# Optimization experiments

Hardware: AMD Instinct MI355X
Metric: run time of the kernel (lower is better)

## Reference

```python
import jax, jax.numpy as jnp
import numpy as np

B = 32768
H = 512
NH = 8
EPS = 1e-5


def _glorot(key, shape):
    fan_in, fan_out = shape[-1], shape[0]
    lim = (6.0 / (fan_in + fan_out)) ** 0.5
    return jax.random.uniform(key, shape, jnp.float32, -lim, lim)


def setup_inputs() -> dict:
    key = jax.random.key(0)
    ks = jax.random.split(key, 32)
    d = {
        "graph_features": jax.random.normal(ks[0], (B, H), jnp.float32),
        "seq_features": jax.random.normal(ks[1], (B, H), jnp.float32),
        "tabular_features": jax.random.normal(ks[2], (B, H), jnp.float32),
    }
    i = 3
    for name in ("g2s", "s2g", "t2m"):
        d[f"{name}_w_in"] = _glorot(ks[i], (3 * H, H)); i += 1
        d[f"{name}_b_in"] = jnp.zeros((3 * H,), jnp.float32)
        d[f"{name}_w_out"] = _glorot(ks[i], (H, H)); i += 1
        d[f"{name}_b_out"] = jnp.zeros((H,), jnp.float32)
    for name in ("gate_g", "gate_s", "gate_t"):
        d[f"{name}_w"] = _glorot(ks[i], (H, 2 * H)); i += 1
        d[f"{name}_b"] = jnp.zeros((H,), jnp.float32)
    d["fc1_w"] = _glorot(ks[i], (2 * H, 3 * H)); i += 1
    d["fc1_b"] = jnp.zeros((2 * H,), jnp.float32)
    d["ln_g"] = jnp.ones((2 * H,), jnp.float32)
    d["ln_b"] = jnp.zeros((2 * H,), jnp.float32)
    d["fc2_w"] = _glorot(ks[i], (H, 2 * H)); i += 1
    d["fc2_b"] = jnp.zeros((H,), jnp.float32)
    return d


def _mha(q, k, v, w_in, b_in, w_out, b_out):
    # q: [B,Sq,H], k/v: [B,Sk,H]. PyTorch nn.MultiheadAttention math (eval mode).
    dh = H // NH
    qp = q @ w_in[:H].T + b_in[:H]
    kp = k @ w_in[H:2 * H].T + b_in[H:2 * H]
    vp = v @ w_in[2 * H:].T + b_in[2 * H:]
    qh = qp.reshape(qp.shape[0], qp.shape[1], NH, dh)
    kh = kp.reshape(kp.shape[0], kp.shape[1], NH, dh)
    vh = vp.reshape(vp.shape[0], vp.shape[1], NH, dh)
    scores = jnp.einsum("bqhd,bkhd->bhqk", qh, kh) / jnp.sqrt(jnp.float32(dh))
    attn = jax.nn.softmax(scores, axis=-1)
    out = jnp.einsum("bhqk,bkhd->bqhd", attn, vh).reshape(q.shape[0], q.shape[1], H)
    return out @ w_out.T + b_out


def reference(graph_features, seq_features, tabular_features,
              g2s_w_in, g2s_b_in, g2s_w_out, g2s_b_out,
              s2g_w_in, s2g_b_in, s2g_w_out, s2g_b_out,
              t2m_w_in, t2m_b_in, t2m_w_out, t2m_b_out,
              gate_g_w, gate_g_b, gate_s_w, gate_s_b, gate_t_w, gate_t_b,
              fc1_w, fc1_b, ln_g, ln_b, fc2_w, fc2_b):
    g = graph_features[:, None, :]   # [B,1,H]
    s = seq_features[:, None, :]
    t = tabular_features[:, None, :]

    graph_to_seq = _mha(s, g, g, g2s_w_in, g2s_b_in, g2s_w_out, g2s_b_out)
    seq_to_graph = _mha(g, s, s, s2g_w_in, s2g_b_in, s2g_w_out, s2g_b_out)

    graph_gate = jax.nn.sigmoid(jnp.concatenate([g, seq_to_graph], -1) @ gate_g_w.T + gate_g_b)
    seq_gate = jax.nn.sigmoid(jnp.concatenate([s, graph_to_seq], -1) @ gate_s_w.T + gate_s_b)
    gated_graph = g * graph_gate
    gated_seq = s * seq_gate

    multimodal = jnp.concatenate([gated_graph, gated_seq], axis=1)  # [B,2,H]
    t2m = _mha(multimodal, t, t, t2m_w_in, t2m_b_in, t2m_w_out, t2m_b_out)  # [B,2,H]

    tab_comb = jnp.concatenate([t, t2m.mean(axis=1, keepdims=True)], -1)
    tab_gate = jax.nn.sigmoid(tab_comb @ gate_t_w.T + gate_t_b)
    gated_tab = t * tab_gate

    allf = jnp.concatenate([gated_graph[:, 0], gated_seq[:, 0], gated_tab[:, 0]], -1)  # [B,3H]
    h = allf @ fc1_w.T + fc1_b
    mu = h.mean(-1, keepdims=True)
    var = ((h - mu) ** 2).mean(-1, keepdims=True)
    h = (h - mu) / jnp.sqrt(var + EPS) * ln_g + ln_b
    h = jax.nn.relu(h)
    return h @ fc2_w.T + fc2_b
```

## Files before the change

### kernel.cpp

```cpp
#include <hip/hip_runtime.h>
#include <stdint.h>
#include <stddef.h>

#define MROWS 32768
#define HDIM  512
#define CH    16384
#define BM 128
#define BN 128
#define BK 64

typedef __attribute__((ext_vector_type(8))) _Float16 half8;
typedef __attribute__((ext_vector_type(4))) _Float16 half4v;
typedef __attribute__((ext_vector_type(4))) float    f32x4;

static __device__ __forceinline__ void gld_lds16(const void* g, void* l) {
    __builtin_amdgcn_global_load_lds(
        (__attribute__((address_space(1))) void*)(uintptr_t)g,
        (__attribute__((address_space(3))) void*)(uint32_t)(uintptr_t)l,
        16, 0, 0);
}

struct CvtJob  { const float* src; _Float16* dst; int srcld4, dstld, rowlen4, rows; };
struct CvtJobs { CvtJob j[11]; };

__global__ __launch_bounds__(256)
void cvt_rows(CvtJobs J) {
    const CvtJob jb = J.j[blockIdx.y];
    const int row = blockIdx.x;
    if (row >= jb.rows) return;
    const float4* __restrict__ s = (const float4*)jb.src + (size_t)row * jb.srcld4;
    _Float16* __restrict__ d = jb.dst + (size_t)row * jb.dstld;
    for (int c = threadIdx.x; c < jb.rowlen4; c += 256) {
        const float4 v = s[c];
        half4v o = { (_Float16)v.x, (_Float16)v.y, (_Float16)v.z, (_Float16)v.w };
        *(half4v*)(d + c * 4) = o;
    }
}

__global__ __launch_bounds__(384)
void cvt_chunk3(const float* __restrict__ x0, const float* __restrict__ x1,
                const float* __restrict__ x2, _Float16* __restrict__ dst) {
    const int row = blockIdx.x;
    const int mod = threadIdx.x >> 7;
    const int c   = threadIdx.x & 127;
    const float* s = (mod == 0) ? x0 : (mod == 1) ? x1 : x2;
    const float4 v = ((const float4*)(s + (size_t)row * 512))[c];
    half4v o = { (_Float16)v.x, (_Float16)v.y, (_Float16)v.z, (_Float16)v.w };
    *(half4v*)(dst + (size_t)row * 1536 + mod * 512 + c * 4) = o;
}

struct TcvtArgs { const float* src[3]; _Float16* dst; };
__global__ __launch_bounds__(256)
void tcvt512(TcvtArgs a) {
    __shared__ float t[32][33];
    const int m = blockIdx.z;
    const float* __restrict__ src = a.src[m];
    _Float16* __restrict__ dst = a.dst + (size_t)m * HDIM * HDIM;
    const int bx = blockIdx.x * 32, by = blockIdx.y * 32;
    const int tx = threadIdx.x & 31, ty = threadIdx.x >> 5;
    #pragma unroll
    for (int q = 0; q < 4; ++q)
        t[ty + q * 8][tx] = src[(size_t)(by + ty + q * 8) * 512 + bx + tx];
    __syncthreads();
    #pragma unroll
    for (int q = 0; q < 4; ++q)
        dst[(size_t)(bx + ty + q * 8) * 512 + by + tx] = (_Float16)t[tx][ty + q * 8];
}

struct MvArgs { const float* W[3]; const float* x[3]; const float* b[3]; float* y; int ldw, woff; };
__global__ __launch_bounds__(256)
void mv3(MvArgs a) {
    const int m = blockIdx.y;
    const int i = blockIdx.x * 256 + threadIdx.x;
    const float* __restrict__ W = a.W[m] + (size_t)i * a.ldw + a.woff;
    const float* __restrict__ x = a.x[m];
    float s = a.b[m][i];
    for (int j = 0; j < 512; ++j) s += W[j] * x[j];
    a.y[m * 512 + i] = s;
}

struct GemmP {
    const void* A1;
    const _Float16* W; const float* bias; void* C;
    int K, ldA1, ldw, ldc, coff;
    int zsA, zsW, zsC;
};

template<int EPI, int OCC>
__global__ __launch_bounds__(256, OCC)
void gemm_k(GemmP p) {
    __shared__ __align__(16) unsigned char smem[32768];
    _Float16* Asm = (_Float16*)smem;
    _Float16* Bsm = (_Float16*)(smem + 16384);

    const int tid  = threadIdx.x;
    const int wid  = tid >> 6;
    const int lane = tid & 63;
    const int m0 = blockIdx.x * BM;
    const int n0 = blockIdx.y * BN;
    const ptrdiff_t zz = (ptrdiff_t)blockIdx.z;
    const _Float16* __restrict__ A1h = (const _Float16*)((const char*)p.A1 + zz * p.zsA);
    const _Float16* __restrict__ Wp  = (const _Float16*)((const char*)p.W + zz * p.zsW);
    char* Cz = (char*)p.C + zz * p.zsC;

    const int wr = (wid >> 1) * 64;
    const int wc = (wid & 1) * 64;
    const int l15 = lane & 15;
    const int lhi = lane >> 4;

    f32x4 acc[4][4] = {};

    for (int kt = 0; kt < p.K; kt += BK) {
        #pragma unroll
        for (int i = 0; i < 4; ++i) {
            const int seg = wid * 256 + i * 64 + lane;
            const int row = seg >> 3;
            const int ke  = (seg & 7) * 8;
            gld_lds16(Wp  + (size_t)(n0 + row) * p.ldw  + kt + ke, &Bsm[seg * 8]);
            gld_lds16(A1h + (size_t)(m0 + row) * p.ldA1 + kt + ke, &Asm[seg * 8]);
        }
        __syncthreads();
        #pragma unroll
        for (int kk = 0; kk < BK; kk += 32) {
            half8 fa[4], fb[4];
            #pragma unroll
            for (int i = 0; i < 4; ++i) {
                fa[i] = *(const half8*)&Asm[(wr + i * 16 + l15) * BK + kk + lhi * 8];
                fb[i] = *(const half8*)&Bsm[(wc + i * 16 + l15) * BK + kk + lhi * 8];
            }
            #pragma unroll
            for (int i = 0; i < 4; ++i)
                #pragma unroll
                for (int j = 0; j < 4; ++j)
                    acc[i][j] = __builtin_amdgcn_mfma_f32_16x16x32_f16(fa[i], fb[j], acc[i][j], 0, 0, 0);
        }
        __syncthreads();
    }

    if (EPI == 3) {
        float* Cf = (float*)smem;
        float* __restrict__ C = (float*)Cz;
        #pragma unroll
        for (int h = 0; h < 2; ++h) {
            if ((wr >> 6) == h) {
                #pragma unroll
                for (int j = 0; j < 4; ++j) {
                    const int col = wc + j * 16 + l15;
                    const float bia = p.bias ? p.bias[n0 + col] : 0.f;
                    #pragma unroll
                    for (int i = 0; i < 4; ++i)
                        #pragma unroll
                        for (int r = 0; r < 4; ++r)
                            Cf[(i * 16 + lhi * 4 + r) * 128 + col] = acc[i][j][r] + bia;
                }
            }
            __syncthreads();
            #pragma unroll
            for (int pph = 0; pph < 8; ++pph) {
                const int seg = pph * 256 + tid;
                const int row = seg >> 5, cs = seg & 31;
                const float4 v = *(const float4*)&Cf[row * 128 + cs * 4];
                *(float4*)&C[(size_t)(m0 + h * 64 + row) * p.ldc + n0 + cs * 4] = v;
            }
            __syncthreads();
        }
    } else {
        _Float16* Ct = (_Float16*)smem;
        #pragma unroll
        for (int j = 0; j < 4; ++j) {
            const int col = wc + j * 16 + l15;
            const float bia = (EPI == 2) ? 0.f : (p.bias ? p.bias[n0 + col] : 0.f);
            #pragma unroll
            for (int i = 0; i < 4; ++i)
                #pragma unroll
                for (int r = 0; r < 4; ++r) {
                    float v = acc[i][j][r] + bia;
                    if (EPI == 1) v = 1.f / (1.f + __expf(-v));
                    Ct[(wr + i * 16 + lhi * 4 + r) * 128 + col] = (_Float16)v;
                }
        }
        __syncthreads();
        _Float16* __restrict__ C = (_Float16*)Cz;
        #pragma unroll
        for (int pph = 0; pph < 8; ++pph) {
            const int seg = pph * 256 + tid;
            const int row = seg >> 4, cs = seg & 15;
            half8 hv = *(const half8*)&Ct[row * 128 + cs * 8];
            const size_t cidx = (size_t)(m0 + row) * p.ldc + p.coff + n0 + cs * 8;
            if (EPI == 1) {
                const half8 xv = *(const half8*)(A1h + (size_t)(m0 + row) * p.ldA1
                                                 + n0 + cs * 8);
                hv = hv * xv;
            }
            if (EPI == 2) { const half8 old = *(const half8*)&C[cidx]; hv = hv + old; }
            *(half8*)&C[cidx] = hv;
        }
    }
}

struct Gemm8P {
    const _Float16* A; const _Float16* W; const float* bias; _Float16* C;
    int K, ldA, ldW, ldc, coff;
};

template<int EPI>
__global__ __launch_bounds__(512, 1)
void gemm8(Gemm8P p) {
    __shared__ __align__(16) unsigned char lds[131072];
    char* LA = (char*)lds;
    char* LB = (char*)lds + 65536;

    const int tid  = threadIdx.x;
    const int wid  = tid >> 6;
    const int lane = tid & 63;
    const int wm = wid >> 2;
    const int wn = wid & 3;
    const int l15 = lane & 15;
    const int lhi = lane >> 4;
    const int m0 = blockIdx.x * 256;
    const int n0 = blockIdx.y * 256;
    const _Float16* __restrict__ A = p.A;
    const _Float16* __restrict__ W = p.W;
    const int ldA = p.ldA, ldW = p.ldW;
    const int nT = p.K >> 6;

    f32x4 acc[8][4] = {};

    auto stage = [&](int t) {
        const int q = t & 1;
        const int kt = t * 64;
        #pragma unroll
        for (int k = 0; k < 4; ++k) {
            const int u = tid + k * 512;
            const int row = u >> 3;
            const int sc = (u & 7) ^ (row & 7);
            gld_lds16(A + (size_t)(m0 + row) * ldA + kt + sc * 8,
                      LA + ((size_t)q * 2048 + u) * 16);
        }
        #pragma unroll
        for (int k = 0; k < 4; ++k) {
            const int u = tid + k * 512;
            const int row = u >> 3;
            const int sc = (u & 7) ^ (row & 7);
            gld_lds16(W + (size_t)(n0 + row) * ldW + kt + sc * 8,
                      LB + ((size_t)q * 2048 + u) * 16);
        }
    };

    stage(0);
    asm volatile("s_waitcnt vmcnt(0)" ::: "memory");
    __builtin_amdgcn_s_barrier();
    asm volatile("" ::: "memory");

    for (int t = 0; t < nT; ++t) {
        const size_t aq = (size_t)(t & 1) * 2048 * 16;
        half8 fb[4][2];
        #pragma unroll
        for (int ph = 0; ph < 4; ++ph) {
            half8 fa[2][2];
            if (ph == 0) {
                #pragma unroll
                for (int nf = 0; nf < 4; ++nf)
                    #pragma unroll
                    for (int kh = 0; kh < 2; ++kh) {
                        const int row = wn * 64 + nf * 16 + l15;
                        const int c16 = (kh * 4 + lhi) ^ (row & 7);
                        fb[nf][kh] = *(const half8*)(LB + aq + ((size_t)row * 8 + c16) * 16);
                    }
            }
            #pragma unroll
            for (int mi = 0; mi < 2; ++mi)
                #pragma unroll
                for (int kh = 0; kh < 2; ++kh) {
                    const int row = wm * 128 + (ph * 2 + mi) * 16 + l15;
                    const int c16 = (kh * 4 + lhi) ^ (row & 7);
                    fa[mi][kh] = *(const half8*)(LA + aq + ((size_t)row * 8 + c16) * 16);
                }
            if (ph == 0 && t + 1 < nT) stage(t + 1);
            asm volatile("" ::: "memory");
            __builtin_amdgcn_s_barrier();
            asm volatile("s_waitcnt lgkmcnt(0)" ::: "memory");
            __builtin_amdgcn_sched_barrier(0);
            __builtin_amdgcn_s_setprio(1);
            #pragma unroll
            for (int mi = 0; mi < 2; ++mi)
                #pragma unroll
                for (int nf = 0; nf < 4; ++nf)
                    #pragma unroll
                    for (int kh = 0; kh < 2; ++kh)
                        acc[ph * 2 + mi][nf] = __builtin_amdgcn_mfma_f32_16x16x32_f16(
                            fa[mi][kh], fb[nf][kh], acc[ph * 2 + mi][nf], 0, 0, 0);
            __builtin_amdgcn_s_setprio(0);
            if (ph == 3) asm volatile("s_waitcnt vmcnt(0)" ::: "memory");
            asm volatile("" ::: "memory");
            __builtin_amdgcn_s_barrier();
            asm volatile("" ::: "memory");
        }
    }

    _Float16* Ct = (_Float16*)lds;
    #pragma unroll
    for (int mf = 0; mf < 8; ++mf)
        #pragma unroll
        for (int nf = 0; nf < 4; ++nf) {
            const int col = wn * 64 + nf * 16 + l15;
            const float bia = p.bias[n0 + col];
            #pragma unroll
            for (int r = 0; r < 4; ++r) {
                float v = acc[mf][nf][r] + bia;
                if (EPI == 1) v = 1.f / (1.f + __expf(-v));
                Ct[(wm * 128 + mf * 16 + lhi * 4 + r) * 256 + col] = (_Float16)v;
            }
        }
    __syncthreads();
    #pragma unroll
    for (int it = 0; it < 16; ++it) {
        const int u = it * 512 + tid;
        const int row = u >> 5, cs = u & 31;
        half8 hv = *(const half8*)&Ct[row * 256 + cs * 8];
        if (EPI == 1) {
            const half8 xv = *(const half8*)(A + (size_t)(m0 + row) * ldA + n0 + cs * 8);
            hv = hv * xv;
        }
        *(half8*)&p.C[(size_t)(m0 + row) * p.ldc + p.coff + n0 + cs * 8] = hv;
    }
}

__global__ __launch_bounds__(256)
void ln_relu(const _Float16* __restrict__ hin, _Float16* __restrict__ hout,
             const float* __restrict__ gamma, const float* __restrict__ beta) {
    const int row  = blockIdx.x * 4 + (threadIdx.x >> 6);
    const int lane = threadIdx.x & 63;
    const _Float16* hr = hin + (size_t)row * 1024;
    _Float16* ho = hout + (size_t)row * 1024;
    const half8 v0 = *(const half8*)(hr + lane * 8);
    const half8 v1 = *(const half8*)(hr + 512 + lane * 8);
    float f0[8], f1[8];
    float s = 0.f, s2 = 0.f;
    #pragma unroll
    for (int j = 0; j < 8; ++j) {
        f0[j] = (float)v0[j]; s += f0[j]; s2 += f0[j] * f0[j];
        f1[j] = (float)v1[j]; s += f1[j]; s2 += f1[j] * f1[j];
    }
    #pragma unroll
    for (int off = 32; off > 0; off >>= 1) {
        s  += __shfl_xor(s,  off, 64);
        s2 += __shfl_xor(s2, off, 64);
    }
    const float mean = s * (1.f / 1024.f);
    const float var  = s2 * (1.f / 1024.f) - mean * mean;
    const float rstd = rsqrtf(var + 1e-5f);
    half8 o0, o1;
    #pragma unroll
    for (int j = 0; j < 8; ++j) {
        const int i0 = lane * 8 + j, i1 = 512 + lane * 8 + j;
        const float av = (f0[j] - mean) * rstd * gamma[i0] + beta[i0];
        const float bv = (f1[j] - mean) * rstd * gamma[i1] + beta[i1];
        o0[j] = (_Float16)(av > 0.f ? av : 0.f);
        o1[j] = (_Float16)(bv > 0.f ? bv : 0.f);
    }
    *(half8*)(ho + lane * 8) = o0;
    *(half8*)(ho + 512 + lane * 8) = o1;
}

extern "C" void kernel_launch(void* const* d_in, const int* in_sizes, int n_in,
                              void* d_out, int out_size, void* d_ws, size_t ws_size,
                              hipStream_t stream)
{
    (void)in_sizes; (void)n_in; (void)out_size;
    const size_t HH = (size_t)HDIM * HDIM;

    _Float16* wsH   = (_Float16*)d_ws;
    _Float16* slotB = wsH;
    _Float16* Xch   = slotB + (size_t)CH * 1536;
    _Float16* Wouth = Xch   + (size_t)CH * 1536;
    _Float16* Wg2h  = Wouth + 3 * HH;
    _Float16* WvT   = Wg2h  + 3 * HH;
    _Float16* WcoT  = WvT   + 3 * HH;
    _Float16* Wbig  = WcoT  + 3 * HH;
    _Float16* Wc2   = Wbig  + 4 * HH;
    _Float16* fc1h  = Wc2   + 1 * HH;
    _Float16* fc2h  = fc1h  + 6 * HH;
    float*    bco   = (float*)(fc2h + 2 * HH);
    float*    beff  = bco + 3 * 512;
    _Float16* hws   = wsH;
    const size_t need = (size_t)((char*)(beff + 3 * 512) - (char*)d_ws);
    if (ws_size < need) return;

    const float* X[3] = { (const float*)d_in[0], (const float*)d_in[1], (const float*)d_in[2] };
    const int asrc[3] = { 1, 0, 2 };

    CvtJobs cj;
    for (int m = 0; m < 3; ++m) {
        cj.j[m]     = { (const float*)d_in[5 + 4 * m], Wouth + m * HH, 128, 512, 128, 512 };
        cj.j[3 + m] = { (const float*)d_in[15 + 2 * m] + 512, Wg2h + m * HH, 256, 512, 128, 512 };
    }
    cj.j[6]  = { (const float*)d_in[15], Wbig,                    256, 1024, 128, 512 };
    cj.j[7]  = { (const float*)d_in[17], Wbig + 512 * 1024 + 512, 256, 1024, 128, 512 };
    cj.j[8]  = { (const float*)d_in[19], Wc2,                     256, 512,  128, 512 };
    cj.j[9]  = { (const float*)d_in[21], fc1h, 384, 1536, 384, 1024 };
    cj.j[10] = { (const float*)d_in[25], fc2h, 256, 1024, 256, 512 };
    cvt_rows<<<dim3(1024, 11, 1), 256, 0, stream>>>(cj);

    TcvtArgs ta;
    for (int m = 0; m < 3; ++m) ta.src[m] = (const float*)d_in[3 + 4 * m] + 2 * HH;
    ta.dst = WvT;
    tcvt512<<<dim3(16, 16, 3), 256, 0, stream>>>(ta);

    MvArgs mv;
    for (int m = 0; m < 3; ++m) {
        mv.W[m] = (const float*)d_in[5 + 4 * m];
        mv.x[m] = (const float*)d_in[4 + 4 * m] + 2 * HDIM;
        mv.b[m] = (const float*)d_in[6 + 4 * m];
    }
    mv.y = bco; mv.ldw = 512; mv.woff = 0;
    mv3<<<dim3(2, 3, 1), 256, 0, stream>>>(mv);

    GemmP p;
    p.bias = nullptr; p.coff = 0;
    p.zsA = p.zsW = p.zsC = 0;

    p.A1 = WvT; p.ldA1 = 512;
    p.W = Wouth; p.ldw = 512;
    p.C = WcoT; p.ldc = 512;
    p.K = 512;
    p.zsA = (int)(HH * 2); p.zsW = (int)(HH * 2); p.zsC = (int)(HH * 2);
    gemm_k<0, 4><<<dim3(4, 4, 3), 256, 0, stream>>>(p);

    p.A1 = Wg2h; p.zsA = (int)(HH * 2);
    p.W = WcoT + HH; p.zsW = -(int)(HH * 2);
    p.C = Wbig + 512; p.ldc = 1024; p.zsC = (int)((512 * 1024 - 512) * 2);
    gemm_k<0, 4><<<dim3(4, 4, 2), 256, 0, stream>>>(p);

    p.A1 = Wg2h + 2 * HH; p.zsA = 0;
    p.W = WcoT + 2 * HH; p.zsW = 0;
    p.C = Wc2; p.ldc = 512; p.zsC = 0;
    gemm_k<2, 4><<<dim3(4, 4, 1), 256, 0, stream>>>(p);

    for (int m = 0; m < 3; ++m) {
        mv.W[m] = (const float*)d_in[15 + 2 * m];
        mv.x[m] = bco + asrc[m] * 512;
        mv.b[m] = (const float*)d_in[16 + 2 * m];
    }
    mv.y = beff; mv.ldw = 1024; mv.woff = 512;
    mv3<<<dim3(2, 3, 1), 256, 0, stream>>>(mv);

    _Float16* hbuf = (_Float16*)d_out;
    Gemm8P g8;
    for (int c = 0; c < 2; ++c) {
        const size_t roff = (size_t)c * CH;

        cvt_chunk3<<<dim3(CH, 1, 1), 384, 0, stream>>>(
            X[0] + roff * HDIM, X[1] + roff * HDIM, X[2] + roff * HDIM, Xch);

        g8.A = Xch; g8.ldA = 1536;
        g8.W = Wbig; g8.ldW = 1024;
        g8.bias = beff;
        g8.C = slotB; g8.ldc = 1536; g8.coff = 0;
        g8.K = 1024;
        gemm8<1><<<dim3(CH / 256, 4, 1), 512, 0, stream>>>(g8);

        p.A1 = Xch + 1024; p.ldA1 = 1536;
        p.W = Wc2; p.ldw = 512;
        p.bias = beff + 1024;
        p.C = slotB; p.ldc = 1536; p.coff = 1024;
        p.K = 512; p.zsA = p.zsW = p.zsC = 0;
        gemm_k<1, 4><<<dim3(CH / BM, 4, 1), 256, 0, stream>>>(p);

        g8.A = slotB; g8.ldA = 1536;
        g8.W = fc1h; g8.ldW = 1536;
        g8.bias = (const float*)d_in[22];
        g8.C = hbuf + roff * 1024; g8.ldc = 1024; g8.coff = 0;
        g8.K = 1536;
        gemm8<0><<<dim3(CH / 256, 4, 1), 512, 0, stream>>>(g8);
    }

    ln_relu<<<dim3(MROWS / 4, 1, 1), 256, 0, stream>>>(
        hbuf, hws, (const float*)d_in[23], (const float*)d_in[24]);

    p.A1 = hws; p.ldA1 = 1024;
    p.W = fc2h; p.ldw = 1024;
    p.bias = (const float*)d_in[26];
    p.C = d_out; p.ldc = HDIM; p.coff = 0;
    p.K = 1024; p.zsA = p.zsW = p.zsC = 0;
    gemm_k<3, 4><<<dim3(MROWS / BM, HDIM / BN, 1), 256, 0, stream>>>(p);
}
```

Baseline: 457.1 us.

## Split K-tiles into half-stages for deeper async LDS prefetch pipeline

Restructures the GEMM main loop so each 64-wide K tile is staged as two 32-wide halves, and the half-tiles are prefetched further ahead (t+1 second half, t+2 first half) with finer-grained vmcnt waits. This is meant to keep more global-to-LDS loads in flight and drop one barrier per phase, hiding memory latency behind the MFMAs. The LDS swizzle changes to a 4-chunk XOR layout for the 32-wide halves, and the fragment reuse pattern changes so B fragments are loaded once per half. It adds intricate wait-count bookkeeping that must match the number of outstanding loads, and removing the pre-compute barrier could race if the counts are off.

```diff
diff --git a/kernel.cpp b/kernel.cpp
--- a/kernel.cpp
+++ b/kernel.cpp
@@ -226,72 +226,71 @@
 
     f32x4 acc[8][4] = {};
 
-    auto stage = [&](int t) {
+    auto stageh = [&](const _Float16* src, int ld, int r0, char* base, int t, int kh) {
         const int q = t & 1;
-        const int kt = t * 64;
-        #pragma unroll
-        for (int k = 0; k < 4; ++k) {
-            const int u = tid + k * 512;
-            const int row = u >> 3;
-            const int sc = (u & 7) ^ (row & 7);
-            gld_lds16(A + (size_t)(m0 + row) * ldA + kt + sc * 8,
-                      LA + ((size_t)q * 2048 + u) * 16);
-        }
-        #pragma unroll
-        for (int k = 0; k < 4; ++k) {
-            const int u = tid + k * 512;
-            const int row = u >> 3;
-            const int sc = (u & 7) ^ (row & 7);
-            gld_lds16(W + (size_t)(n0 + row) * ldW + kt + sc * 8,
-                      LB + ((size_t)q * 2048 + u) * 16);
+        const int kt = t * 64 + kh * 32;
+        char* dst = base + (size_t)(q * 2 + kh) * 16384;
+        #pragma unroll
+        for (int k = 0; k < 2; ++k) {
+            const int j = tid + k * 512;
+            const int row = j >> 2, i = j & 3;
+            const int kc = i ^ ((row >> 1) & 3);
+            gld_lds16(src + (size_t)(r0 + row) * ld + kt + kc * 8,
+                      dst + (size_t)j * 16);
         }
     };
-
-    stage(0);
-    asm volatile("s_waitcnt vmcnt(0)" ::: "memory");
+    #define STAGE8(t, kh) { stageh(A, ldA, m0, LA, (t), (kh)); stageh(W, ldW, n0, LB, (t), (kh)); }
+
+    STAGE8(0, 0);
+    STAGE8(0, 1);
+    if (nT > 1) { STAGE8(1, 0); asm volatile("s_waitcnt vmcnt(8)" ::: "memory"); }
+    else        {               asm volatile("s_waitcnt vmcnt(0)" ::: "memory"); }
     __builtin_amdgcn_s_barrier();
     asm volatile("" ::: "memory");
 
     for (int t = 0; t < nT; ++t) {
-        const size_t aq = (size_t)(t & 1) * 2048 * 16;
-        half8 fb[4][2];
+        const int q = t & 1;
+        half8 fb[4];
         #pragma unroll
         for (int ph = 0; ph < 4; ++ph) {
-            half8 fa[2][2];
-            if (ph == 0) {
+            const int kh = ph >> 1, g = ph & 1;
+            const char* ra = LA + (size_t)(q * 2 + kh) * 16384;
+            const char* rb = LB + (size_t)(q * 2 + kh) * 16384;
+            half8 fa[4];
+            if (g == 0) {
                 #pragma unroll
-                for (int nf = 0; nf < 4; ++nf)
-                    #pragma unroll
-                    for (int kh = 0; kh < 2; ++kh) {
-                        const int row = wn * 64 + nf * 16 + l15;
-                        const int c16 = (kh * 4 + lhi) ^ (row & 7);
-                        fb[nf][kh] = *(const half8*)(LB + aq + ((size_t)row * 8 + c16) * 16);
-                    }
-            }
-            #pragma unroll
-            for (int mi = 0; mi < 2; ++mi)
-                #pragma unroll
-                for (int kh = 0; kh < 2; ++kh) {
-                    const int row = wm * 128 + (ph * 2 + mi) * 16 + l15;
-                    const int c16 = (kh * 4 + lhi) ^ (row & 7);
-                    fa[mi][kh] = *(const half8*)(LA + aq + ((size_t)row * 8 + c16) * 16);
+                for (int nf = 0; nf < 4; ++nf) {
+                    const int row = wn * 64 + nf * 16 + l15;
+                    const int sl = lhi ^ ((row >> 1) & 3);
+                    fb[nf] = *(const half8*)(rb + ((size_t)row * 4 + sl) * 16);
                 }
-            if (ph == 0 && t + 1 < nT) stage(t + 1);
-            asm volatile("" ::: "memory");
-            __builtin_amdgcn_s_barrier();
+            }
+            #pragma unroll
+            for (int mi = 0; mi < 4; ++mi) {
+                const int row = wm * 128 + (g * 4 + mi) * 16 + l15;
+                const int sl = lhi ^ ((row >> 1) & 3);
+                fa[mi] = *(const half8*)(ra + ((size_t)row * 4 + sl) * 16);
+            }
+            if (ph == 0 && t + 1 < nT) STAGE8(t + 1, 1);
+            if (ph == 2 && t + 2 < nT) STAGE8(t + 2, 0);
             asm volatile("s_waitcnt lgkmcnt(0)" ::: "memory");
             __builtin_amdgcn_sched_barrier(0);
             __builtin_amdgcn_s_setprio(1);
             #pragma unroll
-            for (int mi = 0; mi < 2; ++mi)
+            for (int mi = 0; mi < 4; ++mi)
                 #pragma unroll
                 for (int nf = 0; nf < 4; ++nf)
-                    #pragma unroll
-                    for (int kh = 0; kh < 2; ++kh)
-                        acc[ph * 2 + mi][nf] = __builtin_amdgcn_mfma_f32_16x16x32_f16(
-                            fa[mi][kh], fb[nf][kh], acc[ph * 2 + mi][nf], 0, 0, 0);
+                    acc[g * 4 + mi][nf] = __builtin_amdgcn_mfma_f32_16x16x32_f16(
+                        fa[mi], fb[nf], acc[g * 4 + mi][nf], 0, 0, 0);
             __builtin_amdgcn_s_setprio(0);
-            if (ph == 3) asm volatile("s_waitcnt vmcnt(0)" ::: "memory");
+            if (ph == 1) {
+                if (t + 1 < nT) asm volatile("s_waitcnt vmcnt(8)" ::: "memory");
+                else            asm volatile("s_waitcnt vmcnt(0)" ::: "memory");
+            }
+            if (ph == 3) {
+                if (t + 2 < nT)      asm volatile("s_waitcnt vmcnt(8)" ::: "memory");
+                else if (t + 1 < nT) asm volatile("s_waitcnt vmcnt(4)" ::: "memory");
+            }
             asm volatile("" ::: "memory");
             __builtin_amdgcn_s_barrier();
             asm volatile("" ::: "memory");
```

After: 466.2 us. Within noise of the previous version (+2.0%).
